# Performance work log

Measured on AMD Instinct MI355X. Metric: run time of the kernel, lower is better.

The kernel has to match this reference:

```python
import jax, jax.numpy as jnp
import numpy as np

N_NODES = 50000
N_EDGES = 600000
IN_DIM = 128
FEAT = 128
N_CLS = 40


def _lin_params(key, fan_in, fan_out, bias=True):
    k1, k2 = jax.random.split(key)
    lim = 1.0 / np.sqrt(fan_in)
    W = jax.random.uniform(k1, (fan_out, fan_in), jnp.float32, -lim, lim)
    b = jax.random.uniform(k2, (fan_out,), jnp.float32, -lim, lim) if bias else None
    return W, b


def setup_inputs() -> dict:
    key = jax.random.key(0)
    ks = jax.random.split(key, 8)
    x = jax.random.normal(ks[0], (N_NODES, IN_DIM), jnp.float32)
    edge_index = jax.random.randint(ks[1], (2, N_EDGES), 0, N_NODES, jnp.int64 if jax.config.read('jax_enable_x64') else jnp.int32)
    Wl1, bl1 = _lin_params(ks[2], IN_DIM, FEAT)
    Wr1, _ = _lin_params(ks[3], IN_DIM, FEAT, bias=False)
    Wl2, bl2 = _lin_params(ks[4], FEAT, FEAT)
    Wr2, _ = _lin_params(ks[5], FEAT, FEAT, bias=False)
    Wl3, bl3 = _lin_params(ks[6], FEAT, FEAT)
    Wr3, _ = _lin_params(ks[7], FEAT, FEAT, bias=False)
    kc = jax.random.fold_in(key, 99)
    Wc, bc = _lin_params(kc, FEAT, N_CLS)
    return {"x": x, "edge_index": edge_index,
            "Wl1": Wl1, "bl1": bl1, "Wr1": Wr1,
            "Wl2": Wl2, "bl2": bl2, "Wr2": Wr2,
            "Wl3": Wl3, "bl3": bl3, "Wr3": Wr3,
            "Wc": Wc, "bc": bc}


def _sage_relu(x, src, dst, deg_inv, Wl, bl, Wr):
    # mean aggregation over incoming neighbors: gather at src, scatter-add at dst
    agg = jax.ops.segment_sum(x[src], dst, num_segments=N_NODES)  # [N, F]
    agg = agg * deg_inv[:, None]
    out = agg @ Wl.T + bl + x @ Wr.T  # W1*mean(neigh) + W2*x_root
    return jax.nn.relu(out)


def reference(x, edge_index, Wl1, bl1, Wr1, Wl2, bl2, Wr2, Wl3, bl3, Wr3, Wc, bc):
    src, dst = edge_index[0], edge_index[1]
    deg = jax.ops.segment_sum(jnp.ones((src.shape[0],), x.dtype), dst, num_segments=N_NODES)
    deg_inv = 1.0 / jnp.maximum(deg, 1.0)
    local_repr = _sage_relu(x, src, dst, deg_inv, Wl1, bl1, Wr1)
    global_repr = _sage_relu(local_repr, src, dst, deg_inv, Wl2, bl2, Wr2)
    # invariant_feature_extractor: one SAGEConvwithRelu + (eval-mode) dropout + residual
    h = _sage_relu(global_repr, src, dst, deg_inv, Wl3, bl3, Wr3)
    vanilla_if = h + global_repr
    vanilla_pred = vanilla_if @ Wc.T + bc
    return vanilla_pred
```

## Files before the change

### kernel.cpp

```cpp
#include <hip/hip_runtime.h>
#include <hip/hip_bf16.h>

constexpr int N_NODES = 50000;
constexpr int N_EDGES = 600000;
constexpr int D       = 128;
constexpr int N_CLS   = 40;

using bf16x8 = __attribute__((ext_vector_type(8))) short;
using f32x4  = __attribute__((ext_vector_type(4))) float;

__device__ inline unsigned short f2bf(float f) {
    __hip_bfloat16 h = __float2bfloat16(f);
    return __builtin_bit_cast(unsigned short, h);
}
__device__ inline float bf2f(unsigned short u) {
    __hip_bfloat16 h = __builtin_bit_cast(__hip_bfloat16, u);
    return __bfloat162float(h);
}


__global__ void hist_kernel(const int* __restrict__ ei, int* __restrict__ cnt) {
    int e = blockIdx.x * 256 + threadIdx.x;
    if (e < N_EDGES) atomicAdd(&cnt[ei[N_EDGES + e]], 1);
}

__global__ __launch_bounds__(1024) void scan_block_kernel(const int* __restrict__ cnt,
                                                          int* __restrict__ rs,
                                                          int* __restrict__ bsum, int n) {
    __shared__ int t[1024];
    int tid = threadIdx.x;
    int gid = blockIdx.x * 1024 + tid;
    int v = (gid < n) ? cnt[gid] : 0;
    t[tid] = v;
    __syncthreads();
    for (int off = 1; off < 1024; off <<= 1) {
        int u = (tid >= off) ? t[tid - off] : 0;
        __syncthreads();
        t[tid] += u;
        __syncthreads();
    }
    if (gid < n) rs[gid] = t[tid] - v;
    if (tid == 1023) bsum[blockIdx.x] = t[1023];
}

__global__ void scan_sums_kernel(const int* __restrict__ bsum, int* __restrict__ boff, int nblk) {
    __shared__ int t[64];
    int tid = threadIdx.x;
    int v = (tid < nblk) ? bsum[tid] : 0;
    t[tid] = v;
    __syncthreads();
    for (int off = 1; off < 64; off <<= 1) {
        int u = (tid >= off) ? t[tid - off] : 0;
        __syncthreads();
        t[tid] += u;
        __syncthreads();
    }
    if (tid < nblk) boff[tid] = t[tid] - v;
}

__global__ void finalize_kernel(const int* __restrict__ cnt, int* __restrict__ rs,
                                int* __restrict__ cursor, float* __restrict__ dinv,
                                const int* __restrict__ boff) {
    int i = blockIdx.x * 256 + threadIdx.x;
    if (i < N_NODES) {
        int v = rs[i] + boff[i >> 10];
        rs[i] = v;
        cursor[i] = v;
        dinv[i] = 1.0f / fmaxf((float)cnt[i], 1.0f);
        if (i == 0) rs[N_NODES] = N_EDGES;
    }
}

__global__ void scatter_kernel(const int* __restrict__ ei, int* __restrict__ cursor,
                               int* __restrict__ csr) {
    int e = blockIdx.x * 256 + threadIdx.x;
    if (e < N_EDGES) {
        int d = ei[N_EDGES + e];
        int p = atomicAdd(&cursor[d], 1);
        csr[p] = ei[e];
    }
}

__global__ void split_w3_kernel(const float* __restrict__ Wl1, const float* __restrict__ Wr1,
                                const float* __restrict__ Wl2, const float* __restrict__ Wr2,
                                const float* __restrict__ Wl3, const float* __restrict__ Wr3,
                                unsigned short* __restrict__ hi, unsigned short* __restrict__ lo) {
    int layer = blockIdx.x >> 7;
    int idx = (blockIdx.x & 127) * 256 + threadIdx.x;
    int n = idx >> 8, k = idx & 255;
    const float* Wl = (layer == 0) ? Wl1 : (layer == 1) ? Wl2 : Wl3;
    const float* Wr = (layer == 0) ? Wr1 : (layer == 1) ? Wr2 : Wr3;
    float v = (k < 128) ? Wl[n * 128 + k] : Wr[n * 128 + (k - 128)];
    unsigned short h = f2bf(v);
    size_t o = (size_t)layer * 32768 + idx;
    hi[o] = h;
    lo[o] = f2bf(v - bf2f(h));
}

__global__ void split_wc_kernel(const float* __restrict__ Wc,
                                unsigned short* __restrict__ hi, unsigned short* __restrict__ lo) {
    int idx = blockIdx.x * 256 + threadIdx.x;
    int n = idx >> 7, k = idx & 127;
    float v = (n < N_CLS) ? Wc[n * 128 + k] : 0.f;
    unsigned short h = f2bf(v);
    hi[idx] = h;
    lo[idx] = f2bf(v - bf2f(h));
}

__global__ __launch_bounds__(256) void agg_kernel(const float* __restrict__ feat,
                                                  const int* __restrict__ rs,
                                                  const int* __restrict__ csr,
                                                  const float* __restrict__ dinv,
                                                  float* __restrict__ aggn) {
    int wave = threadIdx.x >> 6;
    int lane = threadIdx.x & 63;
    int node = blockIdx.x * 4 + wave;
    if (node >= N_NODES) return;
    int e0 = rs[node], e1 = rs[node + 1];
    int half = lane >> 5;
    int fl = lane & 31;
    float ax = 0.f, ay = 0.f, az = 0.f, aw = 0.f;

    for (int base = e0; base < e1; base += 64) {
        int cnt = min(64, e1 - base);
        int idxv = (lane < cnt) ? csr[base + lane] : 0;
        int cnt2 = cnt & ~1;
        int j = 0;
        for (; j + 8 <= cnt2; j += 8) {
            int s0 = __shfl(idxv, j + half);
            int s1 = __shfl(idxv, j + 2 + half);
            int s2 = __shfl(idxv, j + 4 + half);
            int s3 = __shfl(idxv, j + 6 + half);
            float4 v0 = *(const float4*)&feat[(size_t)s0 * D + fl * 4];
            float4 v1 = *(const float4*)&feat[(size_t)s1 * D + fl * 4];
            float4 v2 = *(const float4*)&feat[(size_t)s2 * D + fl * 4];
            float4 v3 = *(const float4*)&feat[(size_t)s3 * D + fl * 4];
            ax += v0.x + v1.x + v2.x + v3.x;
            ay += v0.y + v1.y + v2.y + v3.y;
            az += v0.z + v1.z + v2.z + v3.z;
            aw += v0.w + v1.w + v2.w + v3.w;
        }
        for (; j < cnt2; j += 2) {
            int s = __shfl(idxv, j + half);
            float4 v = *(const float4*)&feat[(size_t)s * D + fl * 4];
            ax += v.x; ay += v.y; az += v.z; aw += v.w;
        }
        if (j < cnt) {
            int s = __shfl(idxv, j);
            if (half == 0) {
                float4 v = *(const float4*)&feat[(size_t)s * D + fl * 4];
                ax += v.x; ay += v.y; az += v.z; aw += v.w;
            }
        }
    }
    ax += __shfl(ax, lane ^ 32);
    ay += __shfl(ay, lane ^ 32);
    az += __shfl(az, lane ^ 32);
    aw += __shfl(aw, lane ^ 32);
    if (half == 0) {
        float di = dinv[node];
        float4 o; o.x = ax * di; o.y = ay * di; o.z = az * di; o.w = aw * di;
        *(float4*)&aggn[(size_t)node * D + fl * 4] = o;
    }
}

__global__ __launch_bounds__(256) void gemm_mfma_kernel(const float* __restrict__ Aagg,
                                                        const float* __restrict__ Ax,
                                                        const unsigned short* __restrict__ Whi,
                                                        const unsigned short* __restrict__ Wlo,
                                                        const float* __restrict__ bias,
                                                        float* __restrict__ outp, int M) {
    __shared__ __align__(16) unsigned short AhS[64 * 64];
    __shared__ __align__(16) unsigned short AlS[64 * 64];
    __shared__ __align__(16) unsigned short WhS[128 * 64];
    __shared__ __align__(16) unsigned short WlS[128 * 64];
    char* AhB = (char*)AhS;
    char* AlB = (char*)AlS;
    char* WhB = (char*)WhS;
    char* WlB = (char*)WlS;

    int tid = threadIdx.x;
    int lane = tid & 63;
    int wid = tid >> 6;
    int wr = wid >> 1;
    int wc = wid & 1;
    int lr = lane & 15;
    int kg = (lane >> 4) * 8;
    int row0 = blockIdx.x * 64;

    f32x4 acc[2][4];
#pragma unroll
    for (int f = 0; f < 2; ++f)
#pragma unroll
        for (int j = 0; j < 4; ++j) acc[f][j] = (f32x4){0.f, 0.f, 0.f, 0.f};

    for (int kt = 0; kt < 4; ++kt) {
        const float* Asrc = (kt < 2) ? Aagg : Ax;
        int kcol = (kt & 1) * 64;

#pragma unroll
        for (int it = 0; it < 2; ++it) {
            int slot = tid + it * 256;
            int row = slot >> 3;
            int k8 = (slot & 7) * 8;
            int gr = row0 + row;
            if (gr >= M) gr = M - 1;
            const float* p = &Asrc[(size_t)gr * D + kcol + k8];
            float4 v0 = *(const float4*)p;
            float4 v1 = *(const float4*)(p + 4);
            float fv[8] = {v0.x, v0.y, v0.z, v0.w, v1.x, v1.y, v1.z, v1.w};
            union { unsigned short u[8]; uint4 q; } ph, pl;
#pragma unroll
            for (int j = 0; j < 8; ++j) {
                unsigned short h = f2bf(fv[j]);
                ph.u[j] = h;
                pl.u[j] = f2bf(fv[j] - bf2f(h));
            }
            int boff = (row << 7) + (k8 << 1);
            boff ^= (row & 7) << 4;
            *(uint4*)(AhB + boff) = ph.q;
            *(uint4*)(AlB + boff) = pl.q;
        }
#pragma unroll
        for (int it = 0; it < 4; ++it) {
            int slot = tid + it * 256;
            int n = slot >> 3;
            int k8 = (slot & 7) * 8;
            size_t gsrc = (size_t)n * 256 + kt * 64 + k8;
            uint4 h = *(const uint4*)&Whi[gsrc];
            uint4 l = *(const uint4*)&Wlo[gsrc];
            int boff = (n << 7) + (k8 << 1);
            boff ^= (n & 7) << 4;
            *(uint4*)(WhB + boff) = h;
            *(uint4*)(WlB + boff) = l;
        }
        __syncthreads();

#pragma unroll
        for (int ks = 0; ks < 2; ++ks) {
            int kk = ks * 32 + kg;
            bf16x8 ah[2], al[2];
#pragma unroll
            for (int f = 0; f < 2; ++f) {
                int row = wr * 32 + f * 16 + lr;
                int boff = (row << 7) + (kk << 1);
                boff ^= (row & 7) << 4;
                ah[f] = *(const bf16x8*)(AhB + boff);
                al[f] = *(const bf16x8*)(AlB + boff);
            }
            bf16x8 bh[4], bl[4];
#pragma unroll
            for (int j = 0; j < 4; ++j) {
                int n = wc * 64 + j * 16 + lr;
                int boff = (n << 7) + (kk << 1);
                boff ^= (n & 7) << 4;
                bh[j] = *(const bf16x8*)(WhB + boff);
                bl[j] = *(const bf16x8*)(WlB + boff);
            }
#pragma unroll
            for (int f = 0; f < 2; ++f)
#pragma unroll
                for (int j = 0; j < 4; ++j) {
                    acc[f][j] = __builtin_amdgcn_mfma_f32_16x16x32_bf16(ah[f], bh[j], acc[f][j], 0, 0, 0);
                    acc[f][j] = __builtin_amdgcn_mfma_f32_16x16x32_bf16(ah[f], bl[j], acc[f][j], 0, 0, 0);
                    acc[f][j] = __builtin_amdgcn_mfma_f32_16x16x32_bf16(al[f], bh[j], acc[f][j], 0, 0, 0);
                }
        }
        __syncthreads();
    }

#pragma unroll
    for (int f = 0; f < 2; ++f)
#pragma unroll
        for (int j = 0; j < 4; ++j) {
            int c = wc * 64 + j * 16 + lr;
            float b = bias[c];
#pragma unroll
            for (int r = 0; r < 4; ++r) {
                int gr = row0 + wr * 32 + f * 16 + (lane >> 4) * 4 + r;
                if (gr < M) {
                    float v = fmaxf(acc[f][j][r] + b, 0.f);
                    outp[(size_t)gr * D + c] = v;
                }
            }
        }
}

__global__ __launch_bounds__(256) void gemm_cls_kernel(const float* __restrict__ Aagg,
                                                       const float* __restrict__ Ax,
                                                       const unsigned short* __restrict__ Whi,
                                                       const unsigned short* __restrict__ Wlo,
                                                       const float* __restrict__ bias,
                                                       const float* __restrict__ residf,
                                                       const unsigned short* __restrict__ Wch,
                                                       const unsigned short* __restrict__ Wcl,
                                                       const float* __restrict__ bc,
                                                       float* __restrict__ outp, int M) {
    __shared__ __align__(16) char smem[49152];
    char* AhB = smem;
    char* AlB = smem + 8192;
    char* WhB = smem + 16384;
    char* WlB = smem + 32768;

    int tid = threadIdx.x;
    int lane = tid & 63;
    int wid = tid >> 6;
    int wr = wid >> 1;
    int wc = wid & 1;
    int lr = lane & 15;
    int kg = (lane >> 4) * 8;
    int row0 = blockIdx.x * 64;

    f32x4 acc[2][4];
#pragma unroll
    for (int f = 0; f < 2; ++f)
#pragma unroll
        for (int j = 0; j < 4; ++j) acc[f][j] = (f32x4){0.f, 0.f, 0.f, 0.f};

    for (int kt = 0; kt < 4; ++kt) {
        const float* Asrc = (kt < 2) ? Aagg : Ax;
        int kcol = (kt & 1) * 64;
#pragma unroll
        for (int it = 0; it < 2; ++it) {
            int slot = tid + it * 256;
            int row = slot >> 3;
            int k8 = (slot & 7) * 8;
            int gr = row0 + row;
            if (gr >= M) gr = M - 1;
            const float* p = &Asrc[(size_t)gr * D + kcol + k8];
            float4 v0 = *(const float4*)p;
            float4 v1 = *(const float4*)(p + 4);
            float fv[8] = {v0.x, v0.y, v0.z, v0.w, v1.x, v1.y, v1.z, v1.w};
            union { unsigned short u[8]; uint4 q; } ph, pl;
#pragma unroll
            for (int j = 0; j < 8; ++j) {
                unsigned short h = f2bf(fv[j]);
                ph.u[j] = h;
                pl.u[j] = f2bf(fv[j] - bf2f(h));
            }
            int boff = (row << 7) + (k8 << 1);
            boff ^= (row & 7) << 4;
            *(uint4*)(AhB + boff) = ph.q;
            *(uint4*)(AlB + boff) = pl.q;
        }
#pragma unroll
        for (int it = 0; it < 4; ++it) {
            int slot = tid + it * 256;
            int n = slot >> 3;
            int k8 = (slot & 7) * 8;
            size_t gsrc = (size_t)n * 256 + kt * 64 + k8;
            uint4 h = *(const uint4*)&Whi[gsrc];
            uint4 l = *(const uint4*)&Wlo[gsrc];
            int boff = (n << 7) + (k8 << 1);
            boff ^= (n & 7) << 4;
            *(uint4*)(WhB + boff) = h;
            *(uint4*)(WlB + boff) = l;
        }
        __syncthreads();
#pragma unroll
        for (int ks = 0; ks < 2; ++ks) {
            int kk = ks * 32 + kg;
            bf16x8 ah[2], al[2];
#pragma unroll
            for (int f = 0; f < 2; ++f) {
                int row = wr * 32 + f * 16 + lr;
                int boff = (row << 7) + (kk << 1);
                boff ^= (row & 7) << 4;
                ah[f] = *(const bf16x8*)(AhB + boff);
                al[f] = *(const bf16x8*)(AlB + boff);
            }
            bf16x8 bh[4], bl[4];
#pragma unroll
            for (int j = 0; j < 4; ++j) {
                int n = wc * 64 + j * 16 + lr;
                int boff = (n << 7) + (kk << 1);
                boff ^= (n & 7) << 4;
                bh[j] = *(const bf16x8*)(WhB + boff);
                bl[j] = *(const bf16x8*)(WlB + boff);
            }
#pragma unroll
            for (int f = 0; f < 2; ++f)
#pragma unroll
                for (int j = 0; j < 4; ++j) {
                    acc[f][j] = __builtin_amdgcn_mfma_f32_16x16x32_bf16(ah[f], bh[j], acc[f][j], 0, 0, 0);
                    acc[f][j] = __builtin_amdgcn_mfma_f32_16x16x32_bf16(ah[f], bl[j], acc[f][j], 0, 0, 0);
                    acc[f][j] = __builtin_amdgcn_mfma_f32_16x16x32_bf16(al[f], bh[j], acc[f][j], 0, 0, 0);
                }
        }
        __syncthreads();
    }

    f32x4 acc2[3];
#pragma unroll
    for (int j = 0; j < 3; ++j) acc2[j] = (f32x4){0.f, 0.f, 0.f, 0.f};

    for (int p = 0; p < 2; ++p) {
#pragma unroll
        for (int it = 0; it < 2; ++it) {
            int slot = tid + it * 256;
            if (slot < 384) {
                int n = slot >> 3;
                int k8 = (slot & 7) * 8;
                size_t gsrc = (size_t)n * 128 + p * 64 + k8;
                uint4 h = *(const uint4*)&Wch[gsrc];
                uint4 l = *(const uint4*)&Wcl[gsrc];
                int boff = (n << 7) + (k8 << 1);
                boff ^= (n & 7) << 4;
                *(uint4*)(WhB + boff) = h;
                *(uint4*)(WlB + boff) = l;
            }
        }
        if (wc == p) {
#pragma unroll
            for (int f = 0; f < 2; ++f)
#pragma unroll
                for (int j = 0; j < 4; ++j) {
                    int c = wc * 64 + j * 16 + lr;
                    float b = bias[c];
#pragma unroll
                    for (int r = 0; r < 4; ++r) {
                        int row = wr * 32 + f * 16 + (lane >> 4) * 4 + r;
                        int gr = row0 + row;
                        int gra = (gr < M) ? gr : (M - 1);
                        float v = fmaxf(acc[f][j][r] + b, 0.f);
                        v += residf[(size_t)gra * D + c];
                        int kloc = j * 16 + lr;
                        int boff = (row << 7) + (kloc << 1);
                        boff ^= (row & 7) << 4;
                        unsigned short h = f2bf(v);
                        *(unsigned short*)(AhB + boff) = h;
                        *(unsigned short*)(AlB + boff) = f2bf(v - bf2f(h));
                    }
                }
        }
        __syncthreads();

#pragma unroll
        for (int ks = 0; ks < 2; ++ks) {
            int kk = ks * 32 + kg;
            int row = wid * 16 + lr;
            int boffA = (row << 7) + (kk << 1);
            boffA ^= (row & 7) << 4;
            bf16x8 ah = *(const bf16x8*)(AhB + boffA);
            bf16x8 al = *(const bf16x8*)(AlB + boffA);
#pragma unroll
            for (int j = 0; j < 3; ++j) {
                int n = j * 16 + lr;
                int boffB = (n << 7) + (kk << 1);
                boffB ^= (n & 7) << 4;
                bf16x8 bh = *(const bf16x8*)(WhB + boffB);
                bf16x8 bl = *(const bf16x8*)(WlB + boffB);
                acc2[j] = __builtin_amdgcn_mfma_f32_16x16x32_bf16(ah, bh, acc2[j], 0, 0, 0);
                acc2[j] = __builtin_amdgcn_mfma_f32_16x16x32_bf16(ah, bl, acc2[j], 0, 0, 0);
                acc2[j] = __builtin_amdgcn_mfma_f32_16x16x32_bf16(al, bh, acc2[j], 0, 0, 0);
            }
        }
        __syncthreads();
    }

#pragma unroll
    for (int j = 0; j < 3; ++j) {
        int c = j * 16 + lr;
        if (c < N_CLS) {
            float b = bc[c];
#pragma unroll
            for (int r = 0; r < 4; ++r) {
                int gr = row0 + wid * 16 + (lane >> 4) * 4 + r;
                if (gr < M) outp[(size_t)gr * N_CLS + c] = acc2[j][r] + b;
            }
        }
    }
}

extern "C" void kernel_launch(void* const* d_in, const int* in_sizes, int n_in,
                              void* d_out, int out_size, void* d_ws, size_t ws_size,
                              hipStream_t stream) {
    const float* x   = (const float*)d_in[0];
    const int*   ei  = (const int*)d_in[1];
    const float* Wl1 = (const float*)d_in[2];
    const float* bl1 = (const float*)d_in[3];
    const float* Wr1 = (const float*)d_in[4];
    const float* Wl2 = (const float*)d_in[5];
    const float* bl2 = (const float*)d_in[6];
    const float* Wr2 = (const float*)d_in[7];
    const float* Wl3 = (const float*)d_in[8];
    const float* bl3 = (const float*)d_in[9];
    const float* Wr3 = (const float*)d_in[10];
    const float* Wc  = (const float*)d_in[11];
    const float* bc  = (const float*)d_in[12];
    float* out = (float*)d_out;

    char* w = (char*)d_ws;
    size_t off = 0;
    auto carve = [&](size_t bytes) -> void* {
        void* p = w + off;
        off = (off + bytes + 255) & ~(size_t)255;
        return p;
    };
    int*   cnt    = (int*)carve((size_t)N_NODES * 4);
    int*   rs     = (int*)carve((size_t)(N_NODES + 1) * 4);
    int*   cursor = (int*)carve((size_t)N_NODES * 4);
    float* dinv   = (float*)carve((size_t)N_NODES * 4);
    int*   bsum   = (int*)carve(64 * 4);
    int*   boff   = (int*)carve(64 * 4);
    int*   csr    = (int*)carve((size_t)N_EDGES * 4);
    float* aggn   = (float*)carve((size_t)N_NODES * D * 4);
    float* bufA   = (float*)carve((size_t)N_NODES * D * 4);
    float* bufB   = (float*)carve((size_t)N_NODES * D * 4);
    unsigned short* w123h = (unsigned short*)carve(3 * 128 * 256 * 2);
    unsigned short* w123l = (unsigned short*)carve(3 * 128 * 256 * 2);
    unsigned short* wch   = (unsigned short*)carve(48 * 128 * 2);
    unsigned short* wcl   = (unsigned short*)carve(48 * 128 * 2);
    (void)ws_size;

    const int NBLK_SCAN = (N_NODES + 1023) / 1024;
    const int GRID_E = (N_EDGES + 255) / 256;
    const int GRID_N = (N_NODES + 255) / 256;
    const int GRID_AGG = (N_NODES + 3) / 4;
    const int GRID_GEMM = (N_NODES + 63) / 64;

    hipMemsetAsync(cnt, 0, (size_t)N_NODES * 4, stream);
    hipLaunchKernelGGL(hist_kernel, dim3(GRID_E), dim3(256), 0, stream, ei, cnt);
    hipLaunchKernelGGL(split_w3_kernel, dim3(384), dim3(256), 0, stream,
                       Wl1, Wr1, Wl2, Wr2, Wl3, Wr3, w123h, w123l);
    hipLaunchKernelGGL(split_wc_kernel, dim3(24), dim3(256), 0, stream, Wc, wch, wcl);
    hipLaunchKernelGGL(scan_block_kernel, dim3(NBLK_SCAN), dim3(1024), 0, stream, cnt, rs, bsum, N_NODES);
    hipLaunchKernelGGL(scan_sums_kernel, dim3(1), dim3(64), 0, stream, bsum, boff, NBLK_SCAN);
    hipLaunchKernelGGL(finalize_kernel, dim3(GRID_N), dim3(256), 0, stream, cnt, rs, cursor, dinv, boff);
    hipLaunchKernelGGL(scatter_kernel, dim3(GRID_E), dim3(256), 0, stream, ei, cursor, csr);

    hipLaunchKernelGGL(agg_kernel, dim3(GRID_AGG), dim3(256), 0, stream, x, rs, csr, dinv, aggn);
    hipLaunchKernelGGL(gemm_mfma_kernel, dim3(GRID_GEMM), dim3(256), 0, stream,
                       aggn, x, w123h, w123l, bl1, bufA, N_NODES);
    hipLaunchKernelGGL(agg_kernel, dim3(GRID_AGG), dim3(256), 0, stream, bufA, rs, csr, dinv, aggn);
    hipLaunchKernelGGL(gemm_mfma_kernel, dim3(GRID_GEMM), dim3(256), 0, stream,
                       aggn, bufA, w123h + 32768, w123l + 32768, bl2, bufB, N_NODES);
    hipLaunchKernelGGL(agg_kernel, dim3(GRID_AGG), dim3(256), 0, stream, bufB, rs, csr, dinv, aggn);
    hipLaunchKernelGGL(gemm_cls_kernel, dim3(GRID_GEMM), dim3(256), 0, stream,
                       aggn, bufB, w123h + 65536, w123l + 65536, bl3, bufB,
                       wch, wcl, bc, out, N_NODES);
}
```

Baseline: 360.7 us.

## Quantize layer-2 output to int16 for third aggregation and fuse scan finalize

The second GEMM now also writes its ReLU output as fixed-point int16 (scale 2048, clamped), and the third aggregation gathers these half-size rows with integer accumulation before rescaling by the degree inverse. The GEMM K-tile is halved from 64 to 32, which shrinks shared memory but doubles the loop trips and barriers. The separate block-sum scan kernel is folded into the finalize kernel through a wave reduction. The int16 path halves gather traffic for one layer but adds quantization error, saturates values above 16, and costs an extra store in the GEMM epilogue.

```diff
diff --git a/kernel.cpp b/kernel.cpp
--- a/kernel.cpp
+++ b/kernel.cpp
@@ -6,6 +6,9 @@
 constexpr int D       = 128;
 constexpr int N_CLS   = 40;
 
+constexpr float QS = 2048.0f;
+constexpr float DQ = 1.0f / 2048.0f;
+
 using bf16x8 = __attribute__((ext_vector_type(8))) short;
 using f32x4  = __attribute__((ext_vector_type(4))) float;
 
@@ -16,6 +19,11 @@
 __device__ inline float bf2f(unsigned short u) {
     __hip_bfloat16 h = __builtin_bit_cast(__hip_bfloat16, u);
     return __bfloat162float(h);
+}
+__device__ inline short q16(float v) {
+    float s = v * QS;
+    s = fminf(fmaxf(s, -32767.f), 32767.f);
+    return (short)__float2int_rn(s);
 }
 
 
@@ -43,27 +51,22 @@
     if (tid == 1023) bsum[blockIdx.x] = t[1023];
 }
 
-__global__ void scan_sums_kernel(const int* __restrict__ bsum, int* __restrict__ boff, int nblk) {
-    __shared__ int t[64];
+__global__ void finalize2_kernel(const int* __restrict__ cnt, int* __restrict__ rs,
+                                 int* __restrict__ cursor, float* __restrict__ dinv,
+                                 const int* __restrict__ bsum) {
+    __shared__ int chunk_off;
     int tid = threadIdx.x;
-    int v = (tid < nblk) ? bsum[tid] : 0;
-    t[tid] = v;
+    int i = blockIdx.x * 256 + tid;
+    int chunk = blockIdx.x >> 2;
+    if (tid < 64) {
+        int v = (tid < chunk) ? bsum[tid] : 0;
+#pragma unroll
+        for (int o = 1; o < 64; o <<= 1) v += __shfl_xor(v, o);
+        if (tid == 0) chunk_off = v;
+    }
     __syncthreads();
-    for (int off = 1; off < 64; off <<= 1) {
-        int u = (tid >= off) ? t[tid - off] : 0;
-        __syncthreads();
-        t[tid] += u;
-        __syncthreads();
-    }
-    if (tid < nblk) boff[tid] = t[tid] - v;
-}
-
-__global__ void finalize_kernel(const int* __restrict__ cnt, int* __restrict__ rs,
-                                int* __restrict__ cursor, float* __restrict__ dinv,
-                                const int* __restrict__ boff) {
-    int i = blockIdx.x * 256 + threadIdx.x;
     if (i < N_NODES) {
-        int v = rs[i] + boff[i >> 10];
+        int v = rs[i] + chunk_off;
         rs[i] = v;
         cursor[i] = v;
         dinv[i] = 1.0f / fmaxf((float)cnt[i], 1.0f);
@@ -164,16 +167,81 @@
     }
 }
 
+__global__ __launch_bounds__(256) void agg_q_kernel(const short* __restrict__ feat16,
+                                                    const int* __restrict__ rs,
+                                                    const int* __restrict__ csr,
+                                                    const float* __restrict__ dinv,
+                                                    float* __restrict__ aggn) {
+    int wave = threadIdx.x >> 6;
+    int lane = threadIdx.x & 63;
+    int node = blockIdx.x * 4 + wave;
+    if (node >= N_NODES) return;
+    int e0 = rs[node], e1 = rs[node + 1];
+    int q = lane >> 4;
+    int fl = lane & 15;
+    int acc[8] = {0, 0, 0, 0, 0, 0, 0, 0};
+
+    auto acc8 = [&](uint4 u) {
+        acc[0] += (int)(short)(u.x & 0xffff);
+        acc[1] += (int)(short)(u.x >> 16);
+        acc[2] += (int)(short)(u.y & 0xffff);
+        acc[3] += (int)(short)(u.y >> 16);
+        acc[4] += (int)(short)(u.z & 0xffff);
+        acc[5] += (int)(short)(u.z >> 16);
+        acc[6] += (int)(short)(u.w & 0xffff);
+        acc[7] += (int)(short)(u.w >> 16);
+    };
+
+    for (int base = e0; base < e1; base += 64) {
+        int cnt = min(64, e1 - base);
+        int idxv = (lane < cnt) ? csr[base + lane] : 0;
+        int bulk = cnt & ~15;
+        int j = 0;
+        for (; j < bulk; j += 16) {
+            int s0 = __shfl(idxv, j + q);
+            int s1 = __shfl(idxv, j + 4 + q);
+            int s2 = __shfl(idxv, j + 8 + q);
+            int s3 = __shfl(idxv, j + 12 + q);
+            uint4 a = *(const uint4*)&feat16[(size_t)s0 * D + fl * 8];
+            uint4 b = *(const uint4*)&feat16[(size_t)s1 * D + fl * 8];
+            uint4 c = *(const uint4*)&feat16[(size_t)s2 * D + fl * 8];
+            uint4 d = *(const uint4*)&feat16[(size_t)s3 * D + fl * 8];
+            acc8(a); acc8(b); acc8(c); acc8(d);
+        }
+        for (; j < cnt; j += 4) {
+            if (j + q < cnt) {
+                int s = __shfl(idxv, j + q);
+                uint4 a = *(const uint4*)&feat16[(size_t)s * D + fl * 8];
+                acc8(a);
+            }
+        }
+    }
+#pragma unroll
+    for (int i = 0; i < 8; ++i) {
+        acc[i] += __shfl(acc[i], lane ^ 16);
+        acc[i] += __shfl(acc[i], lane ^ 32);
+    }
+    if (q == 0) {
+        float sc = dinv[node] * DQ;
+        float4 o0, o1;
+        o0.x = acc[0] * sc; o0.y = acc[1] * sc; o0.z = acc[2] * sc; o0.w = acc[3] * sc;
+        o1.x = acc[4] * sc; o1.y = acc[5] * sc; o1.z = acc[6] * sc; o1.w = acc[7] * sc;
+        *(float4*)&aggn[(size_t)node * D + fl * 8] = o0;
+        *(float4*)&aggn[(size_t)node * D + fl * 8 + 4] = o1;
+    }
+}
+
 __global__ __launch_bounds__(256) void gemm_mfma_kernel(const float* __restrict__ Aagg,
                                                         const float* __restrict__ Ax,
                                                         const unsigned short* __restrict__ Whi,
                                                         const unsigned short* __restrict__ Wlo,
                                                         const float* __restrict__ bias,
+                                                        short* __restrict__ out16,
                                                         float* __restrict__ outp, int M) {
-    __shared__ __align__(16) unsigned short AhS[64 * 64];
-    __shared__ __align__(16) unsigned short AlS[64 * 64];
-    __shared__ __align__(16) unsigned short WhS[128 * 64];
-    __shared__ __align__(16) unsigned short WlS[128 * 64];
+    __shared__ __align__(16) unsigned short AhS[64 * 32];
+    __shared__ __align__(16) unsigned short AlS[64 * 32];
+    __shared__ __align__(16) unsigned short WhS[128 * 32];
+    __shared__ __align__(16) unsigned short WlS[128 * 32];
     char* AhB = (char*)AhS;
     char* AlB = (char*)AlS;
     char* WhB = (char*)WhS;
@@ -194,15 +262,13 @@
 #pragma unroll
         for (int j = 0; j < 4; ++j) acc[f][j] = (f32x4){0.f, 0.f, 0.f, 0.f};
 
-    for (int kt = 0; kt < 4; ++kt) {
-        const float* Asrc = (kt < 2) ? Aagg : Ax;
-        int kcol = (kt & 1) * 64;
-
-#pragma unroll
-        for (int it = 0; it < 2; ++it) {
-            int slot = tid + it * 256;
-            int row = slot >> 3;
-            int k8 = (slot & 7) * 8;
+    for (int kt = 0; kt < 8; ++kt) {
+        const float* Asrc = (kt < 4) ? Aagg : Ax;
+        int kcol = (kt & 3) * 32;
+
+        {
+            int row = tid >> 2;
+            int k8 = (tid & 3) * 8;
             int gr = row0 + row;
             if (gr >= M) gr = M - 1;
             const float* p = &Asrc[(size_t)gr * D + kcol + k8];
@@ -216,34 +282,32 @@
                 ph.u[j] = h;
                 pl.u[j] = f2bf(fv[j] - bf2f(h));
             }
-            int boff = (row << 7) + (k8 << 1);
+            int boff = (row << 6) + (k8 << 1);
             boff ^= (row & 7) << 4;
             *(uint4*)(AhB + boff) = ph.q;
             *(uint4*)(AlB + boff) = pl.q;
         }
 #pragma unroll
-        for (int it = 0; it < 4; ++it) {
+        for (int it = 0; it < 2; ++it) {
             int slot = tid + it * 256;
-            int n = slot >> 3;
-            int k8 = (slot & 7) * 8;
-            size_t gsrc = (size_t)n * 256 + kt * 64 + k8;
+            int n = slot >> 2;
+            int k8 = (slot & 3) * 8;
+            size_t gsrc = (size_t)n * 256 + kt * 32 + k8;
             uint4 h = *(const uint4*)&Whi[gsrc];
             uint4 l = *(const uint4*)&Wlo[gsrc];
-            int boff = (n << 7) + (k8 << 1);
+            int boff = (n << 6) + (k8 << 1);
             boff ^= (n & 7) << 4;
             *(uint4*)(WhB + boff) = h;
             *(uint4*)(WlB + boff) = l;
         }
         __syncthreads();
 
-#pragma unroll
-        for (int ks = 0; ks < 2; ++ks) {
-            int kk = ks * 32 + kg;
+        {
             bf16x8 ah[2], al[2];
 #pragma unroll
             for (int f = 0; f < 2; ++f) {
                 int row = wr * 32 + f * 16 + lr;
-                int boff = (row << 7) + (kk << 1);
+                int boff = (row << 6) + (kg << 1);
                 boff ^= (row & 7) << 4;
                 ah[f] = *(const bf16x8*)(AhB + boff);
                 al[f] = *(const bf16x8*)(AlB + boff);
@@ -252,7 +316,7 @@
 #pragma unroll
             for (int j = 0; j < 4; ++j) {
                 int n = wc * 64 + j * 16 + lr;
-                int boff = (n << 7) + (kk << 1);
+                int boff = (n << 6) + (kg << 1);
                 boff ^= (n & 7) << 4;
                 bh[j] = *(const bf16x8*)(WhB + boff);
                 bl[j] = *(const bf16x8*)(WlB + boff);
@@ -281,6 +345,7 @@
                 if (gr < M) {
                     float v = fmaxf(acc[f][j][r] + b, 0.f);
                     outp[(size_t)gr * D + c] = v;
+                    if (out16) out16[(size_t)gr * D + c] = q16(v);
                 }
             }
         }
@@ -502,11 +567,11 @@
     int*   cursor = (int*)carve((size_t)N_NODES * 4);
     float* dinv   = (float*)carve((size_t)N_NODES * 4);
     int*   bsum   = (int*)carve(64 * 4);
-    int*   boff   = (int*)carve(64 * 4);
     int*   csr    = (int*)carve((size_t)N_EDGES * 4);
     float* aggn   = (float*)carve((size_t)N_NODES * D * 4);
     float* bufA   = (float*)carve((size_t)N_NODES * D * 4);
     float* bufB   = (float*)carve((size_t)N_NODES * D * 4);
+    short* t16    = (short*)carve((size_t)N_NODES * D * 2);
     unsigned short* w123h = (unsigned short*)carve(3 * 128 * 256 * 2);
     unsigned short* w123l = (unsigned short*)carve(3 * 128 * 256 * 2);
     unsigned short* wch   = (unsigned short*)carve(48 * 128 * 2);
@@ -525,17 +590,16 @@
                        Wl1, Wr1, Wl2, Wr2, Wl3, Wr3, w123h, w123l);
     hipLaunchKernelGGL(split_wc_kernel, dim3(24), dim3(256), 0, stream, Wc, wch, wcl);
     hipLaunchKernelGGL(scan_block_kernel, dim3(NBLK_SCAN), dim3(1024), 0, stream, cnt, rs, bsum, N_NODES);
-    hipLaunchKernelGGL(scan_sums_kernel, dim3(1), dim3(64), 0, stream, bsum, boff, NBLK_SCAN);
-    hipLaunchKernelGGL(finalize_kernel, dim3(GRID_N), dim3(256), 0, stream, cnt, rs, cursor, dinv, boff);
+    hipLaunchKernelGGL(finalize2_kernel, dim3(GRID_N), dim3(256), 0, stream, cnt, rs, cursor, dinv, bsum);
     hipLaunchKernelGGL(scatter_kernel, dim3(GRID_E), dim3(256), 0, stream, ei, cursor, csr);
 
     hipLaunchKernelGGL(agg_kernel, dim3(GRID_AGG), dim3(256), 0, stream, x, rs, csr, dinv, aggn);
     hipLaunchKernelGGL(gemm_mfma_kernel, dim3(GRID_GEMM), dim3(256), 0, stream,
-                       aggn, x, w123h, w123l, bl1, bufA, N_NODES);
+                       aggn, x, w123h, w123l, bl1, (short*)nullptr, bufA, N_NODES);
     hipLaunchKernelGGL(agg_kernel, dim3(GRID_AGG), dim3(256), 0, stream, bufA, rs, csr, dinv, aggn);
     hipLaunchKernelGGL(gemm_mfma_kernel, dim3(GRID_GEMM), dim3(256), 0, stream,
-                       aggn, bufA, w123h + 32768, w123l + 32768, bl2, bufB, N_NODES);
-    hipLaunchKernelGGL(agg_kernel, dim3(GRID_AGG), dim3(256), 0, stream, bufB, rs, csr, dinv, aggn);
+                       aggn, bufA, w123h + 32768, w123l + 32768, bl2, t16, bufB, N_NODES);
+    hipLaunchKernelGGL(agg_q_kernel, dim3(GRID_AGG), dim3(256), 0, stream, t16, rs, csr, dinv, aggn);
     hipLaunchKernelGGL(gemm_cls_kernel, dim3(GRID_GEMM), dim3(256), 0, stream,
                        aggn, bufB, w123h + 65536, w123l + 65536, bl3, bufB,
                        wch, wcl, bc, out, N_NODES);
```

After: 341.4 us. 1.06x faster.
